# Kernel tuning notes

Measured on AMD Instinct MI355X. Metric: run time of the kernel, lower is better.

## Reference

```python
import jax, jax.numpy as jnp
import numpy as np

NH, NP = 4, 4  # num_heads, num_points (num_levels = 1)
LN_EPS = 1e-5


def _layernorm(t, g, b):
    m = t.mean(-1, keepdims=True)
    v = t.var(-1, keepdims=True)
    return (t - m) / jnp.sqrt(v + LN_EPS) * g + b


def setup_inputs() -> dict:
    key = jax.random.key(0)
    ks = jax.random.split(key, 12)
    C, B, H, W = 256, 2, 128, 128
    s = 0.02
    w = lambda k, shape: jax.random.normal(k, shape, jnp.float32) * s
    return {
        "x": jax.random.normal(ks[0], (B, C, H, W), jnp.float32),
        "norm_g": jnp.ones((C,), jnp.float32),
        "norm_b": jnp.zeros((C,), jnp.float32),
        "ffn_g": jnp.ones((C,), jnp.float32),
        "ffn_b": jnp.zeros((C,), jnp.float32),
        "W_val": w(ks[1], (C, C)),
        "b_val": jnp.zeros((C,), jnp.float32),
        "W_off": w(ks[2], (NH * NP * 2, C)),
        "b_off": jax.random.normal(ks[3], (NH * NP * 2,), jnp.float32),
        "W_attn": w(ks[4], (NH * NP, C)),
        "b_attn": jnp.zeros((NH * NP,), jnp.float32),
        "W_out": w(ks[5], (C, C)),
        "b_out": jnp.zeros((C,), jnp.float32),
        "dw_w": w(ks[6], (C, 1, 3, 3)),
        "dw_b": jnp.zeros((C,), jnp.float32),
        "pr_w": w(ks[7], (C, C // 2)),
        "pr_b": jnp.zeros((C,), jnp.float32),
    }


def reference(x, norm_g, norm_b, ffn_g, ffn_b, W_val, b_val, W_off, b_off,
              W_attn, b_attn, W_out, b_out, dw_w, dw_b, pr_w, pr_b):
    B, C, H, W = x.shape
    D = C // NH
    N = H * W
    xf = x.reshape(B, C, N).transpose(0, 2, 1)  # [B, N, C]
    q = _layernorm(xf, norm_g, norm_b)           # query == value (pre-norm)

    value = (q @ W_val.T + b_val).reshape(B, N, NH, D)
    off = (q @ W_off.T + b_off).reshape(B, N, NH, NP, 2)
    aw = jax.nn.softmax((q @ W_attn.T + b_attn).reshape(B, N, NH, NP), axis=-1)

    # reference points: normalized pixel centers (x, y) in [0, 1]
    gx = (jnp.arange(W, dtype=x.dtype) + 0.5) / W
    gy = (jnp.arange(H, dtype=x.dtype) + 0.5) / H
    my, mx = jnp.meshgrid(gy, gx, indexing='ij')
    ref = jnp.stack([mx.reshape(-1), my.reshape(-1)], axis=-1)  # [N, 2]

    offset_norm = jnp.array([W, H], x.dtype)
    loc = ref[None, :, None, None, :] + off / offset_norm  # [B,N,NH,NP,2]

    # grid_sample bilinear, align_corners=False, zero padding
    px = loc[..., 0] * W - 0.5
    py = loc[..., 1] * H - 0.5
    x0 = jnp.floor(px)
    y0 = jnp.floor(py)
    wx = (px - x0).transpose(0, 2, 1, 3)[..., None]  # [B,NH,N,NP,1]
    wy = (py - y0).transpose(0, 2, 1, 3)[..., None]
    x0i = x0.astype(jnp.int32)
    y0i = y0.astype(jnp.int32)

    vt = value.transpose(0, 2, 1, 3)  # [B, NH, N, D]

    def gather(xi, yi):
        valid = ((xi >= 0) & (xi < W) & (yi >= 0) & (yi < H)).astype(x.dtype)
        idx = jnp.clip(yi, 0, H - 1) * W + jnp.clip(xi, 0, W - 1)  # [B,N,NH,NP]
        it = idx.transpose(0, 2, 1, 3).reshape(B, NH, N * NP, 1)
        g = jnp.take_along_axis(vt, it, axis=2).reshape(B, NH, N, NP, D)
        return g * valid.transpose(0, 2, 1, 3)[..., None]

    v00 = gather(x0i, y0i)
    v01 = gather(x0i + 1, y0i)
    v10 = gather(x0i, y0i + 1)
    v11 = gather(x0i + 1, y0i + 1)
    sampled = (v00 * (1 - wx) * (1 - wy) + v01 * wx * (1 - wy)
               + v10 * (1 - wx) * wy + v11 * wx * wy)  # [B,NH,N,NP,D]

    attn_out = (sampled * aw.transpose(0, 2, 1, 3)[..., None]).sum(3)  # [B,NH,N,D]
    attn_out = attn_out.transpose(0, 2, 1, 3).reshape(B, N, C)
    out = attn_out @ W_out.T + b_out + xf  # residual (identity), dropout=0

    res = out
    y = _layernorm(out, ffn_g, ffn_b)
    yi = y.transpose(0, 2, 1).reshape(B, C, H, W)
    dw = jax.lax.conv_general_dilated(
        yi, dw_w, (1, 1), 'SAME', feature_group_count=C,
        dimension_numbers=('NCHW', 'OIHW', 'NCHW')) + dw_b[None, :, None, None]
    x1, x2 = dw[:, :C // 2], dw[:, C // 2:]
    h = jax.nn.silu(x1) * x2  # [B, C/2, H, W]
    pr = jnp.einsum('bchw,oc->bohw', h, pr_w) + pr_b[None, :, None, None]
    return pr + res.transpose(0, 2, 1).reshape(B, C, H, W)
```

## Files before the change

### kernel.cpp

```cpp
#include <hip/hip_runtime.h>
#include <cmath>

typedef unsigned short u16;
typedef __attribute__((ext_vector_type(8))) short short8v;
typedef __attribute__((ext_vector_type(4))) float f32x4;

#define C_DIM 256
#define H_DIM 128
#define W_DIM 128
#define N_DIM (H_DIM*W_DIM)
#define B_DIM 2
#define LN_EPSF 1e-5f

__device__ __forceinline__ u16 f2b(float f) {
  unsigned u = __float_as_uint(f);
  unsigned r = (u + 0x7fffu + ((u >> 16) & 1u)) >> 16;
  return (u16)r;
}
__device__ __forceinline__ float b2f(u16 h) {
  return __uint_as_float(((unsigned)h) << 16);
}

__global__ __launch_bounds__(256) void k_cvt5(const float* __restrict__ w0,
      const float* __restrict__ w1, const float* __restrict__ w2,
      const float* __restrict__ w3, const float* __restrict__ w4,
      u16* __restrict__ d0, u16* __restrict__ d1, u16* __restrict__ d2,
      u16* __restrict__ d3) {
  int i = blockIdx.x*256 + threadIdx.x;
  const float* s; u16* d; int l;
  if (i < 16384)      { s = w0; d = d0;        l = i; }
  else if (i < 32768) { s = w1; d = d1;        l = i - 16384; }
  else if (i < 40960) { s = w2; d = d2;        l = i - 32768; }
  else if (i < 43008) { s = w3; d = d3;        l = i - 40960; }
  else if (i < 44032) { s = w4; d = d3 + 8192; l = i - 43008; }
  else return;
  float4 v = *(const float4*)&s[(size_t)l*4];
  d[l*4+0]=f2b(v.x); d[l*4+1]=f2b(v.y); d[l*4+2]=f2b(v.z); d[l*4+3]=f2b(v.w);
}

__global__ __launch_bounds__(256) void k_fused1(const float* __restrict__ x,
      const float* __restrict__ g, const float* __restrict__ bta,
      const u16* __restrict__ wv, const float* __restrict__ bval,
      const u16* __restrict__ wab, const float* __restrict__ boff,
      const float* __restrict__ battn,
      u16* __restrict__ val, float* __restrict__ off, float* __restrict__ aw) {
  __shared__ float tile[256*33];
  __shared__ float psum[256], psq[256];
  __shared__ float rmean[32], rstd[32];
  __shared__ u16 qls[64*256];
  int t = threadIdx.x;
  int blk = blockIdx.x;
  int b = blk >> 8;
  int n0 = (blk & 255) * 64;
  for (int half = 0; half < 2; ++half) {
    int nh0 = n0 + half*32;
    int nl = t & 31, cr = t >> 5;
    #pragma unroll 4
    for (int i = 0; i < 32; ++i) {
      int c = i*8 + cr;
      tile[c*33 + nl] = x[((size_t)(b*C_DIM + c))*N_DIM + nh0 + nl];
    }
    __syncthreads();
    {
      int n = t & 31, j = t >> 5;
      float s = 0.f, s2 = 0.f;
      #pragma unroll 8
      for (int i = 0; i < 32; ++i) {
        float v = tile[(j*32+i)*33 + n];
        s += v; s2 += v*v;
      }
      psum[j*32+n] = s; psq[j*32+n] = s2;
    }
    __syncthreads();
    if (t < 32) {
      float s=0.f, s2=0.f;
      for (int j=0;j<8;++j){ s += psum[j*32+t]; s2 += psq[j*32+t]; }
      float m = s * (1.f/256.f);
      float var = s2 * (1.f/256.f) - m*m;
      rmean[t] = m; rstd[t] = rsqrtf(var + LN_EPSF);
    }
    __syncthreads();
    float gt = g[t], bt = bta[t];
    #pragma unroll 4
    for (int i = 0; i < 32; ++i) {
      float v = tile[t*33 + i];
      int n = half*32 + i;
      qls[n*256 + (t ^ ((n & 7) << 3))] = f2b((v - rmean[i]) * rstd[i] * gt + bt);
    }
    __syncthreads();
  }
  int lane = t & 63, w = t >> 6;
  int l15 = lane & 15, lk = (lane >> 4) * 8;
  f32x4 acc[4][4] = {};
  f32x4 acc_oa[4] = {};
  float bias_v[4];
  #pragma unroll
  for (int oj = 0; oj < 4; ++oj) bias_v[oj] = bval[w*64 + oj*16 + l15];
  #pragma unroll
  for (int k0 = 0; k0 < 256; k0 += 32) {
    short8v af[4], bf[4];
    #pragma unroll
    for (int mi = 0; mi < 4; ++mi) {
      int n = mi*16 + l15;
      af[mi] = *(const short8v*)&qls[n*256 + ((k0 + lk) ^ ((n & 7) << 3))];
    }
    #pragma unroll
    for (int oj = 0; oj < 4; ++oj)
      bf[oj] = *(const short8v*)&wv[(size_t)(w*64 + oj*16 + l15)*256 + k0 + lk];
    #pragma unroll
    for (int mi = 0; mi < 4; ++mi)
      #pragma unroll
      for (int oj = 0; oj < 4; ++oj)
        acc[mi][oj] = __builtin_amdgcn_mfma_f32_16x16x32_bf16(af[mi], bf[oj], acc[mi][oj], 0,0,0);
    if (w < 3) {
      short8v bw = *(const short8v*)&wab[(size_t)(w*16 + l15)*256 + k0 + lk];
      #pragma unroll
      for (int mi = 0; mi < 4; ++mi)
        acc_oa[mi] = __builtin_amdgcn_mfma_f32_16x16x32_bf16(af[mi], bw, acc_oa[mi], 0,0,0);
    }
  }
  int rbase = (lane >> 4) * 4;
  #pragma unroll
  for (int mi = 0; mi < 4; ++mi)
    #pragma unroll
    for (int oj = 0; oj < 4; ++oj)
      #pragma unroll
      for (int r = 0; r < 4; ++r) {
        size_t m = (size_t)(b*N_DIM + n0 + mi*16 + rbase + r);
        int o = w*64 + oj*16 + l15;
        val[m*256 + o] = f2b(acc[mi][oj][r] + bias_v[oj]);
      }
  if (w < 2) {
    int o = w*16 + l15;
    float bv2 = boff[o];
    #pragma unroll
    for (int mi = 0; mi < 4; ++mi)
      #pragma unroll
      for (int r = 0; r < 4; ++r) {
        size_t m = (size_t)(b*N_DIM + n0 + mi*16 + rbase + r);
        off[m*32 + o] = acc_oa[mi][r] + bv2;
      }
  } else if (w == 2) {
    float bv2 = battn[l15];
    #pragma unroll
    for (int mi = 0; mi < 4; ++mi)
      #pragma unroll
      for (int r = 0; r < 4; ++r) {
        float v = acc_oa[mi][r] + bv2;
        float mx = fmaxf(v, __shfl_xor(v, 1));
        mx = fmaxf(mx, __shfl_xor(mx, 2));
        float e = expf(v - mx);
        float s = e + __shfl_xor(e, 1);
        s = s + __shfl_xor(s, 2);
        size_t m = (size_t)(b*N_DIM + n0 + mi*16 + rbase + r);
        aw[m*16 + l15] = e / s;
      }
  }
}

__global__ __launch_bounds__(256) void k_sample_out(const u16* __restrict__ value,
      const float* __restrict__ off, const float* __restrict__ aw,
      const u16* __restrict__ wo, const float* __restrict__ bo,
      u16* __restrict__ ao) {
  __shared__ u16 sls[64*256];
  int t = threadIdx.x;
  int lane = t & 63, w = t >> 6;
  int blk = blockIdx.x;
  int b = blk >> 8;
  int n0 = (blk & 255) * 64;
  int nh = lane >> 4;
  int dg = (lane & 15) * 4;
  #pragma unroll 1
  for (int it = 0; it < 16; ++it) {
    int rl = it*4 + w;
    int ng = n0 + rl;
    size_t bn = (size_t)b*N_DIM + ng;
    int hc = ng >> 7, wc = ng & 127;
    int vbase = b*(N_DIM*256) + nh*64 + dg;
    const float* op = &off[bn*32 + nh*8];
    const float* ap = &aw[bn*16 + nh*4];
    float acc0=0.f, acc1=0.f, acc2=0.f, acc3=0.f;
    #pragma unroll
    for (int p = 0; p < 4; ++p) {
      float ox = op[p*2+0], oy = op[p*2+1];
      float a  = ap[p];
      float px = (float)wc + ox;
      float py = (float)hc + oy;
      float x0f = floorf(px), y0f = floorf(py);
      float wx = px - x0f, wy = py - y0f;
      int x0 = (int)x0f, y0 = (int)y0f;
      int x1 = x0 + 1, y1 = y0 + 1;
      float fx0 = (1.f - wx) * ((x0 >= 0 && x0 < W_DIM) ? 1.f : 0.f);
      float fx1 = wx         * ((x1 >= 0 && x1 < W_DIM) ? 1.f : 0.f);
      float fy0 = a * (1.f - wy) * ((y0 >= 0 && y0 < H_DIM) ? 1.f : 0.f);
      float fy1 = a * wy         * ((y1 >= 0 && y1 < H_DIM) ? 1.f : 0.f);
      int xc0 = min(max(x0,0),W_DIM-1), xc1 = min(max(x1,0),W_DIM-1);
      int yc0 = min(max(y0,0),H_DIM-1), yc1 = min(max(y1,0),H_DIM-1);
      int r0 = yc0*W_DIM, r1 = yc1*W_DIM;
      {
        ushort4 v = *(const ushort4*)&value[vbase + (r0+xc0)*256];
        float wgt = fx0*fy0;
        acc0 += wgt*b2f(v.x); acc1 += wgt*b2f(v.y); acc2 += wgt*b2f(v.z); acc3 += wgt*b2f(v.w);
      }
      {
        ushort4 v = *(const ushort4*)&value[vbase + (r0+xc1)*256];
        float wgt = fx1*fy0;
        acc0 += wgt*b2f(v.x); acc1 += wgt*b2f(v.y); acc2 += wgt*b2f(v.z); acc3 += wgt*b2f(v.w);
      }
      {
        ushort4 v = *(const ushort4*)&value[vbase + (r1+xc0)*256];
        float wgt = fx0*fy1;
        acc0 += wgt*b2f(v.x); acc1 += wgt*b2f(v.y); acc2 += wgt*b2f(v.z); acc3 += wgt*b2f(v.w);
      }
      {
        ushort4 v = *(const ushort4*)&value[vbase + (r1+xc1)*256];
        float wgt = fx1*fy1;
        acc0 += wgt*b2f(v.x); acc1 += wgt*b2f(v.y); acc2 += wgt*b2f(v.z); acc3 += wgt*b2f(v.w);
      }
    }
    ushort4 o4;
    o4.x = f2b(acc0); o4.y = f2b(acc1); o4.z = f2b(acc2); o4.w = f2b(acc3);
    int k = nh*64 + dg;
    *(ushort4*)&sls[rl*256 + (k ^ ((rl & 7) << 3))] = o4;
  }
  __syncthreads();
  int l15 = lane & 15, lk = (lane >> 4) * 8;
  f32x4 acc[4][4] = {};
  float bias_v[4];
  #pragma unroll
  for (int oj = 0; oj < 4; ++oj) bias_v[oj] = bo[w*64 + oj*16 + l15];
  #pragma unroll
  for (int k0 = 0; k0 < 256; k0 += 32) {
    short8v af[4], bf[4];
    #pragma unroll
    for (int mi = 0; mi < 4; ++mi) {
      int n = mi*16 + l15;
      af[mi] = *(const short8v*)&sls[n*256 + ((k0 + lk) ^ ((n & 7) << 3))];
    }
    #pragma unroll
    for (int oj = 0; oj < 4; ++oj)
      bf[oj] = *(const short8v*)&wo[(size_t)(w*64 + oj*16 + l15)*256 + k0 + lk];
    #pragma unroll
    for (int mi = 0; mi < 4; ++mi)
      #pragma unroll
      for (int oj = 0; oj < 4; ++oj)
        acc[mi][oj] = __builtin_amdgcn_mfma_f32_16x16x32_bf16(af[mi], bf[oj], acc[mi][oj], 0,0,0);
  }
  int rbase = (lane >> 4) * 4;
  #pragma unroll
  for (int mi = 0; mi < 4; ++mi)
    #pragma unroll
    for (int oj = 0; oj < 4; ++oj)
      #pragma unroll
      for (int r = 0; r < 4; ++r) {
        size_t m = (size_t)(b*N_DIM + n0 + mi*16 + rbase + r);
        int o = w*64 + oj*16 + l15;
        ao[m*256 + o] = f2b(acc[mi][oj][r] + bias_v[oj]);
      }
}

__global__ __launch_bounds__(256) void k_ln2res(const u16* __restrict__ ao,
                    const float* __restrict__ x,
                    const float* __restrict__ g, const float* __restrict__ bta,
                    u16* __restrict__ yt, u16* __restrict__ res) {
  __shared__ float tile[256*33];
  __shared__ float psum[256], psq[256];
  __shared__ float rmean[32], rstd[32];
  int t = threadIdx.x;
  int blk = blockIdx.x;
  int b = blk >> 9;
  int n0 = (blk & 511) * 32;
  {
    size_t xb = ((size_t)(b*C_DIM + t))*N_DIM + n0;
    #pragma unroll
    for (int i4 = 0; i4 < 8; ++i4) {
      float4 xv = *(const float4*)&x[xb + i4*4];
      float o0 = b2f(ao[((size_t)(b*N_DIM + n0 + i4*4+0))*C_DIM + t]) + xv.x;
      float o1 = b2f(ao[((size_t)(b*N_DIM + n0 + i4*4+1))*C_DIM + t]) + xv.y;
      float o2 = b2f(ao[((size_t)(b*N_DIM + n0 + i4*4+2))*C_DIM + t]) + xv.z;
      float o3 = b2f(ao[((size_t)(b*N_DIM + n0 + i4*4+3))*C_DIM + t]) + xv.w;
      tile[t*33 + i4*4+0] = o0;
      tile[t*33 + i4*4+1] = o1;
      tile[t*33 + i4*4+2] = o2;
      tile[t*33 + i4*4+3] = o3;
      ushort4 rv; rv.x=f2b(o0); rv.y=f2b(o1); rv.z=f2b(o2); rv.w=f2b(o3);
      *(ushort4*)&res[xb + i4*4] = rv;
    }
  }
  __syncthreads();
  {
    int n = t & 31, j = t >> 5;
    float s = 0.f, s2 = 0.f;
    #pragma unroll 8
    for (int i = 0; i < 32; ++i) {
      float v = tile[(j*32+i)*33 + n];
      s += v; s2 += v*v;
    }
    psum[j*32+n] = s; psq[j*32+n] = s2;
  }
  __syncthreads();
  if (t < 32) {
    float s=0.f, s2=0.f;
    for (int j=0;j<8;++j){ s += psum[j*32+t]; s2 += psq[j*32+t]; }
    float m = s * (1.f/256.f);
    float var = s2 * (1.f/256.f) - m*m;
    rmean[t] = m; rstd[t] = rsqrtf(var + LN_EPSF);
  }
  __syncthreads();
  int nl = t & 31, cr = t >> 5;
  #pragma unroll 4
  for (int i = 0; i < 32; ++i) {
    int c = i*8 + cr;
    float v = tile[c*33 + nl];
    yt[((size_t)(b*C_DIM + c))*N_DIM + n0 + nl] = f2b((v - rmean[nl]) * rstd[nl] * g[c] + bta[c]);
  }
}

__global__ __launch_bounds__(256) void k_dwconv(const u16* __restrict__ yt,
     const float* __restrict__ dww, const float* __restrict__ dwb,
     u16* __restrict__ hb) {
  int t = threadIdx.x;
  int blk = blockIdx.x;
  int ht = blk & 63; int c = (blk >> 6) & 127; int b = blk >> 13;
  int hh = t >> 7; int ww = t & 127;
  int h = ht*2 + hh;
  const u16* p1 = yt + ((size_t)(b*256 + c))*N_DIM;
  const u16* p2 = yt + ((size_t)(b*256 + c + 128))*N_DIM;
  float w1[9], w2[9];
  #pragma unroll
  for (int i=0;i<9;++i){ w1[i]=dww[c*9+i]; w2[i]=dww[(c+128)*9+i]; }
  float a1 = dwb[c], a2 = dwb[c+128];
  #pragma unroll
  for (int ky=0;ky<3;++ky){
    int yy = h + ky - 1;
    if (yy < 0 || yy >= H_DIM) continue;
    #pragma unroll
    for (int kx=0;kx<3;++kx){
      int xx = ww + kx - 1;
      if (xx < 0 || xx >= W_DIM) continue;
      float v1 = b2f(p1[yy*W_DIM+xx]), v2 = b2f(p2[yy*W_DIM+xx]);
      a1 += w1[ky*3+kx]*v1; a2 += w2[ky*3+kx]*v2;
    }
  }
  float sig = 1.f/(1.f+expf(-a1));
  hb[((size_t)(b*128+c))*N_DIM + h*W_DIM + ww] = f2b(a1*sig*a2);
}

__global__ __launch_bounds__(256) void k_prfinal_mfma(const u16* __restrict__ hsrc,
     const u16* __restrict__ pw,
     const float* __restrict__ prb,
     const u16* __restrict__ resb,
     float* __restrict__ dout) {
  __shared__ u16 hls[64*128];
  int t = threadIdx.x;
  int lane = t & 63, w = t >> 6;
  int b = blockIdx.y;
  int n0 = blockIdx.x * 64;
  #pragma unroll
  for (int r = 0; r < 4; ++r) {
    int e = t + 256*r;
    int k = e >> 3;
    int n8 = (e & 7) * 8;
    short8v v = *(const short8v*)&hsrc[((size_t)(b*128 + k))*N_DIM + n0 + n8];
    #pragma unroll
    for (int j = 0; j < 8; ++j) {
      int n = n8 + j;
      hls[n*128 + (k ^ ((n & 7) << 3))] = (u16)v[j];
    }
  }
  __syncthreads();
  int l15 = lane & 15, lk = (lane >> 4) * 8;
  f32x4 acc[4][4] = {};
  #pragma unroll
  for (int k0 = 0; k0 < 128; k0 += 32) {
    short8v af[4], bf[4];
    #pragma unroll
    for (int oi = 0; oi < 4; ++oi)
      af[oi] = *(const short8v*)&pw[(size_t)(w*64 + oi*16 + l15)*128 + k0 + lk];
    #pragma unroll
    for (int nj = 0; nj < 4; ++nj) {
      int n = nj*16 + l15;
      bf[nj] = *(const short8v*)&hls[n*128 + ((k0 + lk) ^ ((n & 7) << 3))];
    }
    #pragma unroll
    for (int oi = 0; oi < 4; ++oi)
      #pragma unroll
      for (int nj = 0; nj < 4; ++nj)
        acc[oi][nj] = __builtin_amdgcn_mfma_f32_16x16x32_bf16(af[oi], bf[nj], acc[oi][nj], 0,0,0);
  }
  int rbase = (lane >> 4) * 4;
  #pragma unroll
  for (int oi = 0; oi < 4; ++oi)
    #pragma unroll
    for (int r = 0; r < 4; ++r) {
      int o = w*64 + oi*16 + rbase + r;
      float pb = prb[o];
      #pragma unroll
      for (int nj = 0; nj < 4; ++nj) {
        int n = n0 + nj*16 + l15;
        size_t idx = ((size_t)(b*256 + o))*N_DIM + n;
        dout[idx] = acc[oi][nj][r] + pb + b2f(resb[idx]);
      }
    }
}

extern "C" void kernel_launch(void* const* d_in, const int* in_sizes, int n_in,
                              void* d_out, int out_size, void* d_ws, size_t ws_size,
                              hipStream_t stream) {
  const float* x      = (const float*)d_in[0];
  const float* norm_g = (const float*)d_in[1];
  const float* norm_b = (const float*)d_in[2];
  const float* ffn_g  = (const float*)d_in[3];
  const float* ffn_b  = (const float*)d_in[4];
  const float* W_val  = (const float*)d_in[5];
  const float* b_val  = (const float*)d_in[6];
  const float* W_off  = (const float*)d_in[7];
  const float* b_off  = (const float*)d_in[8];
  const float* W_attn = (const float*)d_in[9];
  const float* b_attn = (const float*)d_in[10];
  const float* W_out  = (const float*)d_in[11];
  const float* b_out  = (const float*)d_in[12];
  const float* dw_w   = (const float*)d_in[13];
  const float* dw_b   = (const float*)d_in[14];
  const float* pr_w   = (const float*)d_in[15];
  const float* pr_b   = (const float*)d_in[16];
  float* outp = (float*)d_out;

  char* ws = (char*)d_ws;
  const size_t MB = 1u << 20;
  u16*   valbf  = (u16*)(ws);
  u16*   ytbf   = (u16*)(ws);
  u16*   resbf  = (u16*)(ws + 17*MB);
  u16*   aobf   = (u16*)(ws + 34*MB);
  u16*   hbuf   = (u16*)(ws + 34*MB);
  float* boffb  = (float*)(ws + 64*MB);
  float* bawb   = (float*)(ws + 69*MB);
  u16*   wvbf   = (u16*)(ws + 72*MB);
  u16*   wobf   = (u16*)(ws + 72*MB + 131072u);
  u16*   pwbf   = (u16*)(ws + 72*MB + 262144u);
  u16*   wabbf  = (u16*)(ws + 72*MB + 327680u);

  k_cvt5<<<dim3(172), dim3(256), 0, stream>>>(W_val, W_out, pr_w, W_off, W_attn,
                                              wvbf, wobf, pwbf, wabbf);
  k_fused1<<<dim3(512), dim3(256), 0, stream>>>(x, norm_g, norm_b, wvbf, b_val,
                                                wabbf, b_off, b_attn,
                                                valbf, boffb, bawb);
  k_sample_out<<<dim3(512), dim3(256), 0, stream>>>(valbf, boffb, bawb, wobf, b_out, aobf);
  k_ln2res<<<dim3(1024), dim3(256), 0, stream>>>(aobf, x, ffn_g, ffn_b, ytbf, resbf);
  k_dwconv<<<dim3(16384), dim3(256), 0, stream>>>(ytbf, dw_w, dw_b, hbuf);
  k_prfinal_mfma<<<dim3(256, 2), dim3(256), 0, stream>>>(hbuf, pwbf, pr_b, resbf, outp);

  (void)in_sizes; (void)n_in; (void)out_size; (void)ws_size;
}
```

Baseline: 131.0 us.

## Fuse output projection, residual add and FFN LayerNorm into sampling kernel

Merges k_ln2res into the sampling and output-projection kernel. The MFMA accumulators now get the bias and residual x added in registers, and LayerNorm row statistics are reduced across waves through shared memory. Both res and yt are then written directly in channel-major layout. This removes one launch and the bf16 round trip of the attention output through global memory. The cost is strided 4-element x reads and ushort4 stores along N per channel, which may coalesce poorly, plus extra barriers and workspace buffers repositioned to avoid aliasing.

```diff
diff --git a/kernel.cpp b/kernel.cpp
--- a/kernel.cpp
+++ b/kernel.cpp
@@ -158,11 +158,14 @@
   }
 }
 
-__global__ __launch_bounds__(256) void k_sample_out(const u16* __restrict__ value,
+__global__ __launch_bounds__(256) void k_sample_ln(const u16* __restrict__ value,
       const float* __restrict__ off, const float* __restrict__ aw,
       const u16* __restrict__ wo, const float* __restrict__ bo,
-      u16* __restrict__ ao) {
+      const float* __restrict__ x,
+      const float* __restrict__ g, const float* __restrict__ bta,
+      u16* __restrict__ yt, u16* __restrict__ res) {
   __shared__ u16 sls[64*256];
+  __shared__ float rmean[64], rstd[64];
   int t = threadIdx.x;
   int lane = t & 63, w = t >> 6;
   int blk = blockIdx.x;
@@ -225,10 +228,14 @@
   }
   __syncthreads();
   int l15 = lane & 15, lk = (lane >> 4) * 8;
+  int rbase = (lane >> 4) * 4;
   f32x4 acc[4][4] = {};
-  float bias_v[4];
-  #pragma unroll
-  for (int oj = 0; oj < 4; ++oj) bias_v[oj] = bo[w*64 + oj*16 + l15];
+  float bias_v[4], gv[4], btv[4];
+  #pragma unroll
+  for (int oj = 0; oj < 4; ++oj) {
+    int o = w*64 + oj*16 + l15;
+    bias_v[oj] = bo[o]; gv[oj] = g[o]; btv[oj] = bta[o];
+  }
   #pragma unroll
   for (int k0 = 0; k0 < 256; k0 += 32) {
     short8v af[4], bf[4];
@@ -246,74 +253,68 @@
       for (int oj = 0; oj < 4; ++oj)
         acc[mi][oj] = __builtin_amdgcn_mfma_f32_16x16x32_bf16(af[mi], bf[oj], acc[mi][oj], 0,0,0);
   }
-  int rbase = (lane >> 4) * 4;
   #pragma unroll
   for (int mi = 0; mi < 4; ++mi)
     #pragma unroll
-    for (int oj = 0; oj < 4; ++oj)
-      #pragma unroll
-      for (int r = 0; r < 4; ++r) {
-        size_t m = (size_t)(b*N_DIM + n0 + mi*16 + rbase + r);
-        int o = w*64 + oj*16 + l15;
-        ao[m*256 + o] = f2b(acc[mi][oj][r] + bias_v[oj]);
-      }
-}
-
-__global__ __launch_bounds__(256) void k_ln2res(const u16* __restrict__ ao,
-                    const float* __restrict__ x,
-                    const float* __restrict__ g, const float* __restrict__ bta,
-                    u16* __restrict__ yt, u16* __restrict__ res) {
-  __shared__ float tile[256*33];
-  __shared__ float psum[256], psq[256];
-  __shared__ float rmean[32], rstd[32];
-  int t = threadIdx.x;
-  int blk = blockIdx.x;
-  int b = blk >> 9;
-  int n0 = (blk & 511) * 32;
-  {
-    size_t xb = ((size_t)(b*C_DIM + t))*N_DIM + n0;
-    #pragma unroll
-    for (int i4 = 0; i4 < 8; ++i4) {
-      float4 xv = *(const float4*)&x[xb + i4*4];
-      float o0 = b2f(ao[((size_t)(b*N_DIM + n0 + i4*4+0))*C_DIM + t]) + xv.x;
-      float o1 = b2f(ao[((size_t)(b*N_DIM + n0 + i4*4+1))*C_DIM + t]) + xv.y;
-      float o2 = b2f(ao[((size_t)(b*N_DIM + n0 + i4*4+2))*C_DIM + t]) + xv.z;
-      float o3 = b2f(ao[((size_t)(b*N_DIM + n0 + i4*4+3))*C_DIM + t]) + xv.w;
-      tile[t*33 + i4*4+0] = o0;
-      tile[t*33 + i4*4+1] = o1;
-      tile[t*33 + i4*4+2] = o2;
-      tile[t*33 + i4*4+3] = o3;
-      ushort4 rv; rv.x=f2b(o0); rv.y=f2b(o1); rv.z=f2b(o2); rv.w=f2b(o3);
-      *(ushort4*)&res[xb + i4*4] = rv;
-    }
-  }
+    for (int oj = 0; oj < 4; ++oj) {
+      int o = w*64 + oj*16 + l15;
+      const float* xp = &x[((size_t)(b*256 + o))*N_DIM + n0 + mi*16 + rbase];
+      #pragma unroll
+      for (int r = 0; r < 4; ++r)
+        acc[mi][oj][r] += bias_v[oj] + xp[r];
+    }
+  __syncthreads();
+  float* pred = (float*)sls;
+  int cidx = w*16 + l15;
+  #pragma unroll
+  for (int mi = 0; mi < 4; ++mi)
+    #pragma unroll
+    for (int r = 0; r < 4; ++r) {
+      int row = mi*16 + rbase + r;
+      float s  = acc[mi][0][r] + acc[mi][1][r] + acc[mi][2][r] + acc[mi][3][r];
+      float s2 = acc[mi][0][r]*acc[mi][0][r] + acc[mi][1][r]*acc[mi][1][r]
+               + acc[mi][2][r]*acc[mi][2][r] + acc[mi][3][r]*acc[mi][3][r];
+      pred[row*64 + cidx] = s;
+      pred[4096 + row*64 + cidx] = s2;
+    }
   __syncthreads();
   {
-    int n = t & 31, j = t >> 5;
+    int row = t >> 2, q = t & 3;
     float s = 0.f, s2 = 0.f;
-    #pragma unroll 8
-    for (int i = 0; i < 32; ++i) {
-      float v = tile[(j*32+i)*33 + n];
-      s += v; s2 += v*v;
-    }
-    psum[j*32+n] = s; psq[j*32+n] = s2;
+    #pragma unroll
+    for (int i = 0; i < 16; ++i) {
+      s  += pred[row*64 + q*16 + i];
+      s2 += pred[4096 + row*64 + q*16 + i];
+    }
+    s  += __shfl_xor(s, 1);  s  += __shfl_xor(s, 2);
+    s2 += __shfl_xor(s2, 1); s2 += __shfl_xor(s2, 2);
+    if (q == 0) {
+      float m = s * (1.f/256.f);
+      float var = s2 * (1.f/256.f) - m*m;
+      rmean[row] = m; rstd[row] = rsqrtf(var + LN_EPSF);
+    }
   }
   __syncthreads();
-  if (t < 32) {
-    float s=0.f, s2=0.f;
-    for (int j=0;j<8;++j){ s += psum[j*32+t]; s2 += psq[j*32+t]; }
-    float m = s * (1.f/256.f);
-    float var = s2 * (1.f/256.f) - m*m;
-    rmean[t] = m; rstd[t] = rsqrtf(var + LN_EPSF);
-  }
-  __syncthreads();
-  int nl = t & 31, cr = t >> 5;
-  #pragma unroll 4
-  for (int i = 0; i < 32; ++i) {
-    int c = i*8 + cr;
-    float v = tile[c*33 + nl];
-    yt[((size_t)(b*C_DIM + c))*N_DIM + n0 + nl] = f2b((v - rmean[nl]) * rstd[nl] * g[c] + bta[c]);
-  }
+  #pragma unroll
+  for (int mi = 0; mi < 4; ++mi)
+    #pragma unroll
+    for (int oj = 0; oj < 4; ++oj) {
+      int o = w*64 + oj*16 + l15;
+      size_t base = ((size_t)(b*256 + o))*N_DIM + n0 + mi*16 + rbase;
+      ushort4 rv, yv;
+      u16 rr[4], yy[4];
+      #pragma unroll
+      for (int r = 0; r < 4; ++r) {
+        int row = mi*16 + rbase + r;
+        float v = acc[mi][oj][r];
+        rr[r] = f2b(v);
+        yy[r] = f2b((v - rmean[row]) * rstd[row] * gv[oj] + btv[oj]);
+      }
+      rv.x=rr[0]; rv.y=rr[1]; rv.z=rr[2]; rv.w=rr[3];
+      yv.x=yy[0]; yv.y=yy[1]; yv.z=yy[2]; yv.w=yy[3];
+      *(ushort4*)&res[base] = rv;
+      *(ushort4*)&yt[base]  = yv;
+    }
 }
 
 __global__ __launch_bounds__(256) void k_dwconv(const u16* __restrict__ yt,
@@ -347,10 +348,8 @@
 }
 
 __global__ __launch_bounds__(256) void k_prfinal_mfma(const u16* __restrict__ hsrc,
-     const u16* __restrict__ pw,
-     const float* __restrict__ prb,
-     const u16* __restrict__ resb,
-     float* __restrict__ dout) {
+     const u16* __restrict__ pw, const float* __restrict__ prb,
+     const u16* __restrict__ resb, float* __restrict__ dout) {
   __shared__ u16 hls[64*128];
   int t = threadIdx.x;
   int lane = t & 63, w = t >> 6;
@@ -429,10 +428,9 @@
   char* ws = (char*)d_ws;
   const size_t MB = 1u << 20;
   u16*   valbf  = (u16*)(ws);
-  u16*   ytbf   = (u16*)(ws);
   u16*   resbf  = (u16*)(ws + 17*MB);
-  u16*   aobf   = (u16*)(ws + 34*MB);
-  u16*   hbuf   = (u16*)(ws + 34*MB);
+  u16*   ytbf   = (u16*)(ws + 34*MB);
+  u16*   hbuf   = (u16*)(ws + 51*MB);
   float* boffb  = (float*)(ws + 64*MB);
   float* bawb   = (float*)(ws + 69*MB);
   u16*   wvbf   = (u16*)(ws + 72*MB);
@@ -445,8 +443,8 @@
   k_fused1<<<dim3(512), dim3(256), 0, stream>>>(x, norm_g, norm_b, wvbf, b_val,
                                                 wabbf, b_off, b_attn,
                                                 valbf, boffb, bawb);
-  k_sample_out<<<dim3(512), dim3(256), 0, stream>>>(valbf, boffb, bawb, wobf, b_out, aobf);
-  k_ln2res<<<dim3(1024), dim3(256), 0, stream>>>(aobf, x, ffn_g, ffn_b, ytbf, resbf);
+  k_sample_ln<<<dim3(512), dim3(256), 0, stream>>>(valbf, boffb, bawb, wobf, b_out,
+                                                   x, ffn_g, ffn_b, ytbf, resbf);
   k_dwconv<<<dim3(16384), dim3(256), 0, stream>>>(ytbf, dw_w, dw_b, hbuf);
   k_prfinal_mfma<<<dim3(256, 2), dim3(256), 0, stream>>>(hbuf, pwbf, pr_b, resbf, outp);
 
```

New measurement: 134.6 us. +2.8%, slower.
